# Optimization experiments

Hardware: AMD Instinct MI355X
Metric: run time of the kernel (lower is better)

Reference implementation:

```python
import jax, jax.numpy as jnp
import numpy as np

FEATURE_DIM = 512
Z_DIM = 256
Q_DIM = 128
NUM_Z_CODES = 4096
NUM_Q_CODES = 2048
HIDDEN_DIM = 128 * 4  # 512
BOTTLENECK = 64
BATCH = 32768


def setup_inputs() -> dict:
    key = jax.random.key(0)
    ks = jax.random.split(key, 16)
    d = {}
    d['x'] = jax.random.normal(ks[0], (BATCH, FEATURE_DIM), dtype=jnp.float32)
    # encoder: Linear(feature_dim,64) -> GELU -> Linear(64,hidden) -> GELU
    d['eW1'] = jax.random.normal(ks[1], (BOTTLENECK, FEATURE_DIM), dtype=jnp.float32) * (1.0 / np.sqrt(FEATURE_DIM))
    d['eb1'] = jnp.zeros((BOTTLENECK,), jnp.float32)
    d['eW2'] = jax.random.normal(ks[2], (HIDDEN_DIM, BOTTLENECK), dtype=jnp.float32) * (1.0 / np.sqrt(BOTTLENECK))
    d['eb2'] = jnp.zeros((HIDDEN_DIM,), jnp.float32)
    # to_z_latent LipschitzMLP(hidden, z_dim)
    d['zW'] = jax.random.normal(ks[3], (Z_DIM, HIDDEN_DIM), dtype=jnp.float32) * (1.0 / np.sqrt(HIDDEN_DIM))
    d['zb'] = jnp.zeros((Z_DIM,), jnp.float32)
    d['zci'] = jnp.ones((Z_DIM,), jnp.float32)
    # z codebook
    d['z_codebook'] = jax.random.normal(ks[4], (NUM_Z_CODES, Z_DIM), dtype=jnp.float32)
    # q_encoder LipschitzMLP(z_dim, q_dim)
    d['qW'] = jax.random.normal(ks[5], (Q_DIM, Z_DIM), dtype=jnp.float32) * (1.0 / np.sqrt(Z_DIM))
    d['qb'] = jnp.zeros((Q_DIM,), jnp.float32)
    d['qci'] = jnp.ones((Q_DIM,), jnp.float32)
    # q codebook
    d['q_codebook'] = jax.random.normal(ks[6], (NUM_Q_CODES, Q_DIM), dtype=jnp.float32)
    # decoder: Linear(q_dim,64) -> GELU -> Linear(64,hidden) -> GELU
    d['dW1'] = jax.random.normal(ks[7], (BOTTLENECK, Q_DIM), dtype=jnp.float32) * (1.0 / np.sqrt(Q_DIM))
    d['db1'] = jnp.zeros((BOTTLENECK,), jnp.float32)
    d['dW2'] = jax.random.normal(ks[8], (HIDDEN_DIM, BOTTLENECK), dtype=jnp.float32) * (1.0 / np.sqrt(BOTTLENECK))
    d['db2'] = jnp.zeros((HIDDEN_DIM,), jnp.float32)
    # to_output Linear(hidden, feature_dim)
    d['oW'] = jax.random.normal(ks[9], (FEATURE_DIM, HIDDEN_DIM), dtype=jnp.float32) * (1.0 / np.sqrt(HIDDEN_DIM))
    d['ob'] = jnp.zeros((FEATURE_DIM,), jnp.float32)
    return d


def _gelu(x):
    return jax.nn.gelu(x, approximate=False)  # torch nn.GELU default (erf)


def _lipschitz_mlp(x, W, b, ci):
    # normalization: scale each row of W so its L1 norm <= softplus(ci)
    absrowsum = jnp.sum(jnp.abs(W), axis=1, keepdims=True)          # [out,1]
    scale = jnp.minimum(1.0, jax.nn.softplus(ci)[:, None] / absrowsum)
    W_norm = W * scale
    return jax.nn.sigmoid(x @ W_norm.T + b)


def _quantize(z_e, codebook):
    # ||a-b||^2 = ||a||^2 + ||b||^2 - 2 a.b ; single big GEMM
    z_norm = jnp.sum(z_e * z_e, axis=1, keepdims=True)              # [B,1]
    cb_norm = jnp.sum(codebook * codebook, axis=1)[None, :]         # [1,K]
    dists = z_norm + cb_norm - 2.0 * (z_e @ codebook.T)             # [B,K]
    idx = jnp.argmin(dists, axis=1)
    z_q = codebook[idx]
    return z_q, idx


def _mse(a, b):
    return jnp.mean((a - b) ** 2)


def reference(x, eW1, eb1, eW2, eb2, zW, zb, zci, z_codebook,
              qW, qb, qci, q_codebook, dW1, db1, dW2, db2, oW, ob):
    sg = jax.lax.stop_gradient
    # encoder
    h = _gelu(_gelu(x @ eW1.T + eb1) @ eW2.T + eb2)                 # [B,hidden]
    z_e = _lipschitz_mlp(h, zW, zb, zci)                            # [B,z_dim]
    z_q, z_idx = _quantize(z_e, z_codebook)
    commit_z = _mse(z_e, sg(z_q))
    codebook_z = _mse(z_q, sg(z_e))
    # q level
    q_e = _lipschitz_mlp(sg(z_q), qW, qb, qci)                      # [B,q_dim]
    q_q, q_idx = _quantize(q_e, q_codebook)
    commit_q = _mse(q_e, sg(q_q))
    codebook_q = _mse(q_q, sg(q_e))
    # decoder
    dec_h = _gelu(_gelu(q_q @ dW1.T + db1) @ dW2.T + db2)           # [B,hidden]
    x_recon = dec_h @ oW.T + ob                                     # [B,feature]
    recon_loss = _mse(x_recon, x)
    loss = recon_loss + 0.25 * (commit_z + codebook_z) + 0.25 * (commit_q + codebook_q)
    return (loss, recon_loss, commit_z, codebook_z, commit_q, codebook_q,
            x_recon, z_q, q_q, z_idx, q_idx)
```

## Files before the change

### kernel.cpp

```cpp
#include <hip/hip_runtime.h>

typedef unsigned long long u64;
typedef unsigned short u16;
typedef unsigned int u32;


namespace {

constexpr int kBatch = 32768;

__device__ __forceinline__ float gelu_f(float x) {
  return 0.5f * x * (1.0f + erff(x * 0.70710678118654752440f));
}
__device__ __forceinline__ float sigmoid_f(float x) {
  return 1.0f / (1.0f + expf(-x));
}
__device__ __forceinline__ u64 pack_key(float d, unsigned j) {
  unsigned u = __float_as_uint(d);
  u = (u & 0x80000000u) ? ~u : (u | 0x80000000u);
  return ((u64)u << 32) | j;
}
__device__ __forceinline__ u16 bf16_rne(float x) {
  unsigned u = __float_as_uint(x);
  unsigned r = (u + 0x7FFFu + ((u >> 16) & 1u)) >> 16;
  return (u16)r;
}
__device__ __forceinline__ float bf16_to_f(u16 h) {
  return __uint_as_float((unsigned)h << 16);
}
__device__ __forceinline__ u64 min64(u64 a, u64 b) { return a < b ? a : b; }

__device__ __forceinline__ void load_lds16(const void* g, void* l) {
  __builtin_amdgcn_global_load_lds(
      (const __attribute__((address_space(1))) void*)g,
      (__attribute__((address_space(3))) void*)l, 16, 0, 0);
}

template <int N>
__device__ __forceinline__ void wait_vmcnt() {
  if constexpr (N == 0) {
    asm volatile("s_waitcnt vmcnt(0)" ::: "memory");
  } else if constexpr (N == 1) {
    asm volatile("s_waitcnt vmcnt(1)" ::: "memory");
  } else if constexpr (N == 2) {
    asm volatile("s_waitcnt vmcnt(2)" ::: "memory");
  } else if constexpr (N == 8) {
    asm volatile("s_waitcnt vmcnt(8)" ::: "memory");
  } else if constexpr (N == 16) {
    asm volatile("s_waitcnt vmcnt(16)" ::: "memory");
  }
}

__device__ __forceinline__ void lds_fence_barrier_pre() {
  asm volatile("s_waitcnt lgkmcnt(0)" ::: "memory");
  __builtin_amdgcn_sched_barrier(0);
  __builtin_amdgcn_s_barrier();
  asm volatile("" ::: "memory");
  __builtin_amdgcn_sched_barrier(0);
}

__device__ __forceinline__ void barrier_raw() {
  __builtin_amdgcn_sched_barrier(0);
  __builtin_amdgcn_s_barrier();
  asm volatile("" ::: "memory");
  __builtin_amdgcn_sched_barrier(0);
}

typedef short bf16x8 __attribute__((ext_vector_type(8)));
typedef float f32x4 __attribute__((ext_vector_type(4)));

__global__ void prep_cb_kernel(const float* __restrict__ zcb,
                               u16* __restrict__ zcbh, float* __restrict__ zcbn,
                               const float* __restrict__ qcb,
                               u16* __restrict__ qcbh, float* __restrict__ qcbn) {
  int b = blockIdx.x;
  const float* cb;
  u16* cbh;
  float* cbn;
  int K;
  if (b < 1024) { cb = zcb; cbh = zcbh; cbn = zcbn; K = 256; }
  else { b -= 1024; cb = qcb; cbh = qcbh; cbn = qcbn; K = 128; }
  const int row = b * 4 + (threadIdx.x >> 6);
  const int lane = threadIdx.x & 63;
  double s = 0.0;
  for (int k = lane; k < K; k += 64) {
    const float v = cb[(size_t)row * K + k];
    cbh[(size_t)row * K + k] = bf16_rne(v);
    s += (double)v * (double)v;
  }
#pragma unroll
  for (int o = 32; o > 0; o >>= 1) s += __shfl_down(s, o);
  if (lane == 0) cbn[row] = (float)s;
}

__global__ void prep_w_kernel(
    const float* __restrict__ zW, const float* __restrict__ zci,
    const float* __restrict__ qW, const float* __restrict__ qci,
    const float* __restrict__ eW1, const float* __restrict__ eW2,
    u16* __restrict__ zWns, u16* __restrict__ qWns, u16* __restrict__ eW1s,
    u16* __restrict__ eW2s, const float* __restrict__ dW1,
    const float* __restrict__ dW2, const float* __restrict__ oW,
    u16* __restrict__ dW1b, u16* __restrict__ dW2b, u16* __restrict__ oWb) {
  const int b = blockIdx.x;
  const int tid = threadIdx.x;
  if (b < 384) {
    const float* W;
    const float* ci;
    u16* D;
    int K, row;
    if (b < 256) { W = zW; ci = zci; D = zWns; K = 512; row = b; }
    else { W = qW; ci = qci; D = qWns; K = 256; row = b - 256; }
    float s = 0.f;
    for (int k = tid; k < K; k += 256) s += fabsf(W[(size_t)row * K + k]);
#pragma unroll
    for (int o = 32; o > 0; o >>= 1) s += __shfl_down(s, o);
    __shared__ float p[4];
    if ((tid & 63) == 0) p[tid >> 6] = s;
    __syncthreads();
    const float tot = p[0] + p[1] + p[2] + p[3];
    const float c = ci[row];
    const float sp = (c > 20.f) ? c : log1pf(expf(c));
    const float scale = fminf(1.f, sp / tot);
    for (int k = tid; k < K; k += 256) {
      const float v = W[(size_t)row * K + k] * scale;
      const u16 h = bf16_rne(v);
      const u16 l = bf16_rne(v - bf16_to_f(h));
      D[(size_t)row * 3 * K + k] = h;
      D[(size_t)row * 3 * K + K + k] = h;
      D[(size_t)row * 3 * K + 2 * K + k] = l;
    }
  } else if (b < 512) {
    const int i = (b - 384) * 256 + tid;
    const int r = i >> 9, k = i & 511;
    const float v = eW1[i];
    const u16 h = bf16_rne(v);
    const u16 l = bf16_rne(v - bf16_to_f(h));
    eW1s[(size_t)r * 1536 + k] = h;
    eW1s[(size_t)r * 1536 + 512 + k] = h;
    eW1s[(size_t)r * 1536 + 1024 + k] = l;
  } else if (b < 640) {
    const int i = (b - 512) * 256 + tid;
    const int r = i >> 6, k = i & 63;
    const float v = eW2[i];
    const u16 h = bf16_rne(v);
    const u16 l = bf16_rne(v - bf16_to_f(h));
    eW2s[(size_t)r * 192 + k] = h;
    eW2s[(size_t)r * 192 + 64 + k] = h;
    eW2s[(size_t)r * 192 + 128 + k] = l;
  } else if (b < 672) {
    const int i = (b - 640) * 256 + tid;
    dW1b[i] = bf16_rne(dW1[i]);
  } else if (b < 800) {
    const int i = (b - 672) * 256 + tid;
    dW2b[i] = bf16_rne(dW2[i]);
  } else {
    const int i = (b - 800) * 256 + tid;
    oWb[i] = bf16_rne(oW[i]);
  }
}

__global__ void cast_split_x_kernel(const float* __restrict__ x,
                                    u16* __restrict__ xs) {
  const int i = blockIdx.x * 256 + threadIdx.x;
  const int row = i >> 7, c4 = i & 127;
  const float4 v = *(const float4*)(x + (size_t)row * 512 + c4 * 4);
  const float vv[4] = {v.x, v.y, v.z, v.w};
  u16 hv[4], lv[4];
#pragma unroll
  for (int j = 0; j < 4; ++j) {
    hv[j] = bf16_rne(vv[j]);
    lv[j] = bf16_rne(vv[j] - bf16_to_f(hv[j]));
  }
  *(ushort4*)(xs + (size_t)row * 1024 + c4 * 4) =
      make_ushort4(hv[0], hv[1], hv[2], hv[3]);
  *(ushort4*)(xs + (size_t)row * 1024 + 512 + c4 * 4) =
      make_ushort4(lv[0], lv[1], lv[2], lv[3]);
}

enum { U_GELU_SPLIT = 0, U_SIG_SPLIT = 1, U_GELU_B16 = 2, U_RECON = 3 };

template <int TM, int TN, int NW, int MODE>
__global__ __launch_bounds__(NW * 64) void gemm_uni(
    const u16* __restrict__ A, const u16* __restrict__ B,
    const float* __restrict__ bias, void* __restrict__ Cv,
    const float* __restrict__ X, float* __restrict__ psum, int Ktot,
    int wrapA, int strideA, int N) {
  __shared__ __align__(16) u16 As[TM * 64];
  __shared__ __align__(16) u16 Bs[TN * 64];
  constexpr int NT = NW * 64;
  constexpr int AIT = (TM * 8) / NT;
  constexpr int BIT = (TN * 8) / NT;
  const int tid = threadIdx.x;
  const int lane = tid & 63, w = tid >> 6;
  const int quad = lane >> 4, l15 = lane & 15;
  const int waveM = (TN == 64) ? w * 64 : (w & 1) * 64;
  const int waveN = (TN == 64) ? 0 : (w >> 1) * 64;
  const int rowBase = blockIdx.y * TM;
  const int colBase = blockIdx.x * TN;

  f32x4 acc[4][4] = {};

  for (int k0 = 0; k0 < Ktot; k0 += 64) {
    const int sk0 = (k0 >= wrapA) ? k0 - wrapA : k0;
    __syncthreads();
#pragma unroll
    for (int i = 0; i < AIT; ++i) {
      const int ch = i * NT + tid;
      const int r = ch >> 3, c = ch & 7, g = c ^ (r & 7);
      load_lds16(A + (size_t)(rowBase + r) * strideA + sk0 + g * 8,
                 (char*)As + ch * 16);
    }
#pragma unroll
    for (int i = 0; i < BIT; ++i) {
      const int ch = i * NT + tid;
      const int r = ch >> 3, c = ch & 7, g = c ^ (r & 7);
      load_lds16(B + (size_t)(colBase + r) * Ktot + k0 + g * 8,
                 (char*)Bs + ch * 16);
    }
    __syncthreads();
#pragma unroll
    for (int ks = 0; ks < 2; ++ks) {
      bf16x8 af[4], bf[4];
      const int ch = ks * 4 + quad;
#pragma unroll
      for (int mi = 0; mi < 4; ++mi) {
        const int rl = waveM + mi * 16 + l15;
        af[mi] = *(const bf16x8*)(As + rl * 64 + (ch ^ (rl & 7)) * 8);
      }
#pragma unroll
      for (int ni = 0; ni < 4; ++ni) {
        const int rl = waveN + ni * 16 + l15;
        bf[ni] = *(const bf16x8*)(Bs + rl * 64 + (ch ^ (rl & 7)) * 8);
      }
#pragma unroll
      for (int mi = 0; mi < 4; ++mi)
#pragma unroll
        for (int ni = 0; ni < 4; ++ni)
          acc[mi][ni] = __builtin_amdgcn_mfma_f32_16x16x32_bf16(
              af[mi], bf[ni], acc[mi][ni], 0, 0, 0);
    }
  }

  if constexpr (MODE == U_GELU_SPLIT || MODE == U_SIG_SPLIT) {
    u16* S = (u16*)Cv;
#pragma unroll
    for (int mi = 0; mi < 4; ++mi)
#pragma unroll
      for (int r = 0; r < 4; ++r) {
        const int row = rowBase + waveM + mi * 16 + quad * 4 + r;
#pragma unroll
        for (int ni = 0; ni < 4; ++ni) {
          const int col = colBase + waveN + ni * 16 + l15;
          const float pre = acc[mi][ni][r] + bias[col];
          const float v = (MODE == U_GELU_SPLIT) ? gelu_f(pre) : sigmoid_f(pre);
          const u16 h = bf16_rne(v);
          const u16 l = bf16_rne(v - bf16_to_f(h));
          S[(size_t)row * 2 * N + col] = h;
          S[(size_t)row * 2 * N + N + col] = l;
        }
      }
  } else if constexpr (MODE == U_GELU_B16) {
    u16* C = (u16*)Cv;
#pragma unroll
    for (int mi = 0; mi < 4; ++mi)
#pragma unroll
      for (int r = 0; r < 4; ++r) {
        const int row = rowBase + waveM + mi * 16 + quad * 4 + r;
#pragma unroll
        for (int ni = 0; ni < 4; ++ni) {
          const int col = colBase + waveN + ni * 16 + l15;
          C[(size_t)row * N + col] =
              bf16_rne(gelu_f(acc[mi][ni][r] + bias[col]));
        }
      }
  } else {
    float* C = (float*)Cv;
    float local = 0.f;
#pragma unroll
    for (int mi = 0; mi < 4; ++mi)
#pragma unroll
      for (int r = 0; r < 4; ++r) {
        const int row = rowBase + waveM + mi * 16 + quad * 4 + r;
#pragma unroll
        for (int ni = 0; ni < 4; ++ni) {
          const int col = colBase + waveN + ni * 16 + l15;
          const float val = acc[mi][ni][r] + bias[col];
          const float d = val - X[(size_t)row * N + col];
          local += d * d;
          C[(size_t)row * N + col] = val;
        }
      }
#pragma unroll
    for (int o = 32; o > 0; o >>= 1) local += __shfl_down(local, o);
    __shared__ float psh[NW];
    if (lane == 0) psh[w] = local;
    __syncthreads();
    if (tid == 0) {
      float t = 0.f;
#pragma unroll
      for (int i = 0; i < NW; ++i) t += psh[i];
      psum[blockIdx.y * gridDim.x + blockIdx.x] = t;
    }
  }
}

template <int KT, int CT, int BR, int BTG>
__global__ __launch_bounds__(256) void dist3z_kernel(
    const u16* __restrict__ CB, const u16* __restrict__ ZB,
    const float* __restrict__ cbn, u32* __restrict__ cand, int strideB,
    int ncand) {
  constexpr int CH = KT / 8;
  constexpr int KSTEPS = KT / 32;
  constexpr int CSLOTS = (CT * CH) / 256;
  constexpr int BSLOTS = (BR * CH) / 256;
  __shared__ __align__(16) u16 bufC[CT * KT];
  __shared__ __align__(16) u16 bufB[BR * KT];
  const int tid = threadIdx.x;
  const int lane = tid & 63, w = tid >> 6;
  const int quad = lane >> 4, l15 = lane & 15;
  const int waveN = w * 32;
  const int ct = blockIdx.y;
  const int btg = blockIdx.x;
  const int codeBase = ct * CT;

  float cnf[2][4];
#pragma unroll
  for (int mi = 0; mi < 2; ++mi)
#pragma unroll
    for (int r = 0; r < 4; ++r)
      cnf[mi][r] =
          cbn[codeBase + mi * 16 + quad * 4 + r] * 512.0f + 131072.0f;
  asm volatile("" ::: "memory");

#pragma unroll
  for (int i = 0; i < CSLOTS; ++i) {
    const int ch = i * 256 + tid;
    const int r = ch / CH, c = ch % CH, g = c ^ (r & 7);
    load_lds16(CB + (size_t)(codeBase + r) * KT + g * 8, (char*)bufC + ch * 16);
  }
  {
    const int rowBase0 = btg * BTG * BR;
#pragma unroll
    for (int i = 0; i < BSLOTS; ++i) {
      const int ch = i * 256 + tid;
      const int r = ch / CH, c = ch % CH, g = c ^ (r & 7);
      load_lds16(ZB + (size_t)(rowBase0 + r) * strideB + g * 8,
                 (char*)bufB + ch * 16);
    }
  }
  wait_vmcnt<0>();
  barrier_raw();

  bf16x8 af[KSTEPS][2];
#pragma unroll
  for (int kk = 0; kk < KSTEPS; ++kk)
#pragma unroll
    for (int mi = 0; mi < 2; ++mi) {
      const int rl = mi * 16 + l15;
      const int sw = (kk * 4 + quad) ^ (rl & 7);
      af[kk][mi] = *(const bf16x8*)(bufC + rl * KT + sw * 8);
    }

#pragma unroll 1
  for (int bt = 0; bt < BTG; ++bt) {
    const int rowBase = (btg * BTG + bt) * BR;

    f32x4 acc[2][2] = {};
#pragma unroll
    for (int kk = 0; kk < KSTEPS; ++kk) {
      bf16x8 bf[2];
#pragma unroll
      for (int ni = 0; ni < 2; ++ni) {
        const int rn = waveN + ni * 16 + l15;
        const int sw = (kk * 4 + quad) ^ (rn & 7);
        bf[ni] = *(const bf16x8*)(bufB + rn * KT + sw * 8);
      }
#pragma unroll
      for (int mi = 0; mi < 2; ++mi)
#pragma unroll
        for (int ni = 0; ni < 2; ++ni)
          acc[mi][ni] = __builtin_amdgcn_mfma_f32_16x16x32_bf16(
              af[kk][mi], bf[ni], acc[mi][ni], 0, 0, 0);
    }

    u32 best[2];
#pragma unroll
    for (int ni = 0; ni < 2; ++ni) {
      u32 b0 = ~0u;
#pragma unroll
      for (int mi = 0; mi < 2; ++mi)
#pragma unroll
        for (int r = 0; r < 4; ++r) {
          const float kf = fmaf(acc[mi][ni][r], -1024.0f, cnf[mi][r]);
          u32 iv = (u32)kf;
          iv = iv > 0xFFFFFu ? 0xFFFFFu : iv;
          const u32 key = (iv << 12) | (codeBase + mi * 16 + quad * 4 + r);
          b0 = min(b0, key);
        }
      b0 = min(b0, (u32)__shfl_xor(b0, 16));
      b0 = min(b0, (u32)__shfl_xor(b0, 32));
      best[ni] = b0;
    }
    lds_fence_barrier_pre();

    if (bt + 1 < BTG) {
      const int rowBaseN = rowBase + BR;
#pragma unroll
      for (int i = 0; i < BSLOTS; ++i) {
        const int ch = i * 256 + tid;
        const int r = ch / CH, c = ch % CH, g = c ^ (r & 7);
        load_lds16(ZB + (size_t)(rowBaseN + r) * strideB + g * 8,
                   (char*)bufB + ch * 16);
      }
    }
    if (quad == 0) {
#pragma unroll
      for (int ni = 0; ni < 2; ++ni) {
        const int row = rowBase + waveN + ni * 16 + l15;
        cand[(size_t)row * ncand + ct] = best[ni];
      }
    }
    wait_vmcnt<2>();
    barrier_raw();
  }
}

template <int KT, int CT, int BR, int BTG>
__global__ __launch_bounds__(256) void dist2z_kernel(
    const u16* __restrict__ CB, const u16* __restrict__ ZB,
    const float* __restrict__ cbn, u32* __restrict__ cand, int strideB,
    int ncand) {
  constexpr int CH = KT / 8;
  constexpr int KSTEPS = KT / 32;
  constexpr int CSLOTS = (CT * CH) / 256;
  constexpr int BSLOTS = (BR * CH) / 256;
  __shared__ __align__(16) u16 bufC[CT * KT];
  __shared__ __align__(16) u16 bufB[BR * KT];
  __shared__ u32 wred[BR * 2];
  const int tid = threadIdx.x;
  const int lane = tid & 63, w = tid >> 6;
  const int quad = lane >> 4, l15 = lane & 15;
  const int waveM = (w & 1) * 32;
  const int waveN = (w >> 1) * 32;
  const int ct = blockIdx.y;
  const int btg = blockIdx.x;
  const int codeBase = ct * CT;

  float cnf[2][4];
#pragma unroll
  for (int mi = 0; mi < 2; ++mi)
#pragma unroll
    for (int r = 0; r < 4; ++r)
      cnf[mi][r] =
          cbn[codeBase + waveM + mi * 16 + quad * 4 + r] * 512.0f + 131072.0f;
  asm volatile("" ::: "memory");

#pragma unroll
  for (int i = 0; i < CSLOTS; ++i) {
    const int ch = i * 256 + tid;
    const int r = ch / CH, c = ch % CH, g = c ^ (r & 7);
    load_lds16(CB + (size_t)(codeBase + r) * KT + g * 8, (char*)bufC + ch * 16);
  }
  {
    const int rowBase0 = btg * BTG * BR;
#pragma unroll
    for (int i = 0; i < BSLOTS; ++i) {
      const int ch = i * 256 + tid;
      const int r = ch / CH, c = ch % CH, g = c ^ (r & 7);
      load_lds16(ZB + (size_t)(rowBase0 + r) * strideB + g * 8,
                 (char*)bufB + ch * 16);
    }
  }
  wait_vmcnt<0>();
  barrier_raw();

  bf16x8 af[KSTEPS][2];
#pragma unroll
  for (int kk = 0; kk < KSTEPS; ++kk)
#pragma unroll
    for (int mi = 0; mi < 2; ++mi) {
      const int rl = waveM + mi * 16 + l15;
      const int sw = (kk * 4 + quad) ^ (rl & 7);
      af[kk][mi] = *(const bf16x8*)(bufC + rl * KT + sw * 8);
    }

#pragma unroll 1
  for (int bt = 0; bt < BTG; ++bt) {
    const int rowBase = (btg * BTG + bt) * BR;

    f32x4 acc[2][2] = {};
#pragma unroll
    for (int kk = 0; kk < KSTEPS; ++kk) {
      bf16x8 bf[2];
#pragma unroll
      for (int ni = 0; ni < 2; ++ni) {
        const int rn = waveN + ni * 16 + l15;
        const int sw = (kk * 4 + quad) ^ (rn & 7);
        bf[ni] = *(const bf16x8*)(bufB + rn * KT + sw * 8);
      }
#pragma unroll
      for (int mi = 0; mi < 2; ++mi)
#pragma unroll
        for (int ni = 0; ni < 2; ++ni)
          acc[mi][ni] = __builtin_amdgcn_mfma_f32_16x16x32_bf16(
              af[kk][mi], bf[ni], acc[mi][ni], 0, 0, 0);
    }

#pragma unroll
    for (int ni = 0; ni < 2; ++ni) {
      u32 b0 = ~0u;
#pragma unroll
      for (int mi = 0; mi < 2; ++mi)
#pragma unroll
        for (int r = 0; r < 4; ++r) {
          const float kf = fmaf(acc[mi][ni][r], -1024.0f, cnf[mi][r]);
          u32 iv = (u32)kf;
          iv = iv > 0xFFFFFu ? 0xFFFFFu : iv;
          const u32 key =
              (iv << 12) | (codeBase + waveM + mi * 16 + quad * 4 + r);
          b0 = min(b0, key);
        }
      b0 = min(b0, (u32)__shfl_xor(b0, 16));
      b0 = min(b0, (u32)__shfl_xor(b0, 32));
      if (quad == 0) {
        const int rloc = waveN + ni * 16 + l15;
        wred[rloc * 2 + (w & 1)] = b0;
      }
    }
    lds_fence_barrier_pre();

    if (bt + 1 < BTG) {
      const int rowBaseN = rowBase + BR;
#pragma unroll
      for (int i = 0; i < BSLOTS; ++i) {
        const int ch = i * 256 + tid;
        const int r = ch / CH, c = ch % CH, g = c ^ (r & 7);
        load_lds16(ZB + (size_t)(rowBaseN + r) * strideB + g * 8,
                   (char*)bufB + ch * 16);
      }
    }
    if (tid < BR) {
      const u32 m0 = min(wred[tid * 2 + 0], wred[tid * 2 + 1]);
      cand[(size_t)(rowBase + tid) * ncand + ct] = m0;
    }
    wait_vmcnt<1>();
    lds_fence_barrier_pre();
  }
}

template <int K, int NC, int LEVEL>
__global__ __launch_bounds__(256, 4) void rerank_kernel(
    const u32* __restrict__ cand, const u16* __restrict__ zes,
    const float* __restrict__ cb, const float* __restrict__ cbn,
    float* __restrict__ outq, u16* __restrict__ wsq,
    float* __restrict__ out_idx, float* __restrict__ psum) {
  constexpr int DV = K / 32;
  constexpr int MV = K / 64;
  constexpr int NK = (NC + 63) / 64;
  const int w = threadIdx.x >> 6, lane = threadIdx.x & 63;
  const int row = blockIdx.x * 4 + w;
  const int g = lane >> 3, sub = lane & 7;

  const u16* zr = zes + (size_t)row * 2 * K;

  ushort4 zh[DV], zl[DV];
#pragma unroll
  for (int i = 0; i < DV; ++i) {
    zh[i] = *(const ushort4*)(zr + sub * (K / 8) + 4 * i);
    zl[i] = *(const ushort4*)(zr + K + sub * (K / 8) + 4 * i);
  }
  float zmse[MV];
#pragma unroll
  for (int i = 0; i < MV; ++i) {
    const int c = lane + 64 * i;
    zmse[i] = bf16_to_f(zr[c]) + bf16_to_f(zr[K + c]);
  }
  u32 mk0 = (lane < NC) ? cand[(size_t)row * NC + lane] : ~0u;
  u32 mk1 = (NK == 2) ? cand[(size_t)row * NC + 64 + lane] : ~0u;

  unsigned topcode[8];
#pragma unroll
  for (int t = 0; t < 8; ++t) {
    u32 m = min(mk0, mk1);
#pragma unroll
    for (int off = 1; off < 64; off <<= 1) m = min(m, (u32)__shfl_xor(m, off));
    topcode[t] = m & 0xFFFu;
    if (mk0 == m) mk0 = ~0u;
    else if (mk1 == m) mk1 = ~0u;
  }
  unsigned ci = topcode[0];
#pragma unroll
  for (int t = 1; t < 8; ++t) ci = (g == t) ? topcode[t] : ci;

  const float* cr = cb + (size_t)ci * K;
  float dot = 0.f;
#pragma unroll
  for (int i = 0; i < DV; ++i) {
    const float4 cv = *(const float4*)(cr + sub * (K / 8) + 4 * i);
    dot = fmaf(bf16_to_f(zh[i].x) + bf16_to_f(zl[i].x), cv.x, dot);
    dot = fmaf(bf16_to_f(zh[i].y) + bf16_to_f(zl[i].y), cv.y, dot);
    dot = fmaf(bf16_to_f(zh[i].z) + bf16_to_f(zl[i].z), cv.z, dot);
    dot = fmaf(bf16_to_f(zh[i].w) + bf16_to_f(zl[i].w), cv.w, dot);
  }
#pragma unroll
  for (int off = 1; off < 8; off <<= 1) dot += __shfl_xor(dot, off);
  u64 k2 = pack_key(cbn[ci] - 2.0f * dot, ci);
#pragma unroll
  for (int off = 8; off < 64; off <<= 1) k2 = min64(k2, __shfl_xor(k2, off));
  const unsigned best = (unsigned)k2;
  if (lane == 0) out_idx[row] = (float)best;

  const float* br = cb + (size_t)best * K;
  float local = 0.f;
#pragma unroll
  for (int i = 0; i < MV; ++i) {
    const int c = lane + 64 * i;
    const float v = br[c];
    const float d = zmse[i] - v;
    local += d * d;
    outq[(size_t)row * K + c] = v;
    if (LEVEL == 0) {
      const u16 h = bf16_rne(v);
      wsq[(size_t)row * 2 * K + c] = h;
      wsq[(size_t)row * 2 * K + K + c] = bf16_rne(v - bf16_to_f(h));
    } else {
      wsq[(size_t)row * K + c] = bf16_rne(v);
    }
  }
#pragma unroll
  for (int o = 32; o > 0; o >>= 1) local += __shfl_down(local, o);
  __shared__ float p[4];
  if (lane == 0) p[w] = local;
  __syncthreads();
  if (threadIdx.x == 0) psum[blockIdx.x] = p[0] + p[1] + p[2] + p[3];
}

__global__ void finalize_kernel(const float* __restrict__ psumZ,
                                const float* __restrict__ psumQ,
                                const float* __restrict__ psumR,
                                float* __restrict__ out) {
  const int tid = threadIdx.x;
  float sz = 0.f, sq = 0.f, sr = 0.f;
  for (int i = tid; i < 8192; i += 256) {
    sz += psumZ[i];
    sq += psumQ[i];
  }
  for (int i = tid; i < 1024; i += 256) sr += psumR[i];
#pragma unroll
  for (int o = 32; o > 0; o >>= 1) {
    sz += __shfl_down(sz, o);
    sq += __shfl_down(sq, o);
    sr += __shfl_down(sr, o);
  }
  __shared__ float pz[4], pq[4], pr[4];
  if ((tid & 63) == 0) {
    pz[tid >> 6] = sz;
    pq[tid >> 6] = sq;
    pr[tid >> 6] = sr;
  }
  __syncthreads();
  if (tid == 0) {
    const float cz = (pz[0] + pz[1] + pz[2] + pz[3]) / ((float)kBatch * 256.f);
    const float cq = (pq[0] + pq[1] + pq[2] + pq[3]) / ((float)kBatch * 128.f);
    const float rec = (pr[0] + pr[1] + pr[2] + pr[3]) / ((float)kBatch * 512.f);
    out[0] = rec + 0.5f * cz + 0.5f * cq;
    out[1] = rec;
    out[2] = cz;
    out[3] = cz;
    out[4] = cq;
    out[5] = cq;
  }
}

}

extern "C" void kernel_launch(void* const* d_in, const int* in_sizes, int n_in,
                              void* d_out, int out_size, void* d_ws,
                              size_t ws_size, hipStream_t stream) {
  const float* x   = (const float*)d_in[0];
  const float* eW1 = (const float*)d_in[1];
  const float* eb1 = (const float*)d_in[2];
  const float* eW2 = (const float*)d_in[3];
  const float* eb2 = (const float*)d_in[4];
  const float* zW  = (const float*)d_in[5];
  const float* zb  = (const float*)d_in[6];
  const float* zci = (const float*)d_in[7];
  const float* zcb = (const float*)d_in[8];
  const float* qW  = (const float*)d_in[9];
  const float* qb  = (const float*)d_in[10];
  const float* qci = (const float*)d_in[11];
  const float* qcb = (const float*)d_in[12];
  const float* dW1 = (const float*)d_in[13];
  const float* db1 = (const float*)d_in[14];
  const float* dW2 = (const float*)d_in[15];
  const float* db2 = (const float*)d_in[16];
  const float* oW  = (const float*)d_in[17];
  const float* ob  = (const float*)d_in[18];

  float* out = (float*)d_out;
  float* out_xr = out + 6;
  float* out_zq = out_xr + (size_t)32768 * 512;
  float* out_qq = out_zq + (size_t)32768 * 256;
  float* out_zi = out_qq + (size_t)32768 * 128;
  float* out_qi = out_zi + 32768;

  char* wsb = (char*)d_ws;
  u16*  zWns = (u16*) (wsb + 0x0000000);
  u16*  qWns = (u16*) (wsb + 0x00C0000);
  u16*  eW1s = (u16*) (wsb + 0x00F0000);
  u16*  eW2s = (u16*) (wsb + 0x0120000);
  u16*  dW1b = (u16*) (wsb + 0x0150000);
  u16*  dW2b = (u16*) (wsb + 0x0154000);
  u16*  oWb  = (u16*) (wsb + 0x0164000);
  u16*  zcbh = (u16*) (wsb + 0x01E4000);
  u16*  qcbh = (u16*) (wsb + 0x03E4000);
  float* zcbn = (float*)(wsb + 0x0464000);
  float* qcbn = (float*)(wsb + 0x0468000);
  float* psumR = (float*)(wsb + 0x046B000);
  float* psumZ = (float*)(wsb + 0x0470000);
  float* psumQ = (float*)(wsb + 0x0478000);
  u16*  h1s  = (u16*) (wsb + 0x0480000);
  u16*  h1b  = (u16*) (wsb + 0x0480000);
  u16*  zes  = (u16*) (wsb + 0x0C80000);
  u16*  qes  = (u16*) (wsb + 0x0C80000);
  u16*  hb   = (u16*) (wsb + 0x0C80000);
  u16*  xs   = (u16*) (wsb + 0x2C80000);
  u16*  hs   = (u16*) (wsb + 0x2C80000);
  u32*  candq = (u32*)(wsb + 0x2C80000);
  u16*  zqs  = (u16*) (wsb + 0x3480000);
  u16*  qqb  = (u16*) (wsb + 0x5480000);
  u32*  candz = (u32*)(wsb + 0x5C80000);

  prep_cb_kernel<<<1536, 256, 0, stream>>>(zcb, zcbh, zcbn, qcb, qcbh, qcbn);
  prep_w_kernel<<<1824, 256, 0, stream>>>(zW, zci, qW, qci, eW1, eW2, zWns,
                                          qWns, eW1s, eW2s, dW1, dW2, oW,
                                          dW1b, dW2b, oWb);
  cast_split_x_kernel<<<16384, 256, 0, stream>>>(x, xs);

  gemm_uni<128, 64, 2, U_GELU_SPLIT><<<dim3(1, 256), 128, 0, stream>>>(
      xs, eW1s, eb1, h1s, nullptr, nullptr, 1536, 1024, 1024, 64);
  gemm_uni<128, 128, 4, U_GELU_SPLIT><<<dim3(4, 256), 256, 0, stream>>>(
      h1s, eW2s, eb2, hs, nullptr, nullptr, 192, 128, 128, 512);
  gemm_uni<128, 128, 4, U_SIG_SPLIT><<<dim3(2, 256), 256, 0, stream>>>(
      hs, zWns, zb, zes, nullptr, nullptr, 1536, 1024, 1024, 256);

  dist3z_kernel<256, 32, 128, 32><<<dim3(8, 128), 256, 0, stream>>>(
      zcbh, zes, zcbn, candz, 512, 128);
  rerank_kernel<256, 128, 0><<<8192, 256, 0, stream>>>(
      candz, zes, zcb, zcbn, out_zq, zqs, out_zi, psumZ);

  gemm_uni<128, 128, 4, U_SIG_SPLIT><<<dim3(1, 256), 256, 0, stream>>>(
      zqs, qWns, qb, qes, nullptr, nullptr, 768, 512, 512, 128);
  dist2z_kernel<128, 64, 64, 16><<<dim3(32, 32), 256, 0, stream>>>(
      qcbh, qes, qcbn, candq, 256, 32);
  rerank_kernel<128, 32, 1><<<8192, 256, 0, stream>>>(
      candq, qes, qcb, qcbn, out_qq, qqb, out_qi, psumQ);

  gemm_uni<128, 64, 2, U_GELU_B16><<<dim3(1, 256), 128, 0, stream>>>(
      qqb, dW1b, db1, h1b, nullptr, nullptr, 128, 1 << 30, 128, 64);
  gemm_uni<128, 128, 4, U_GELU_B16><<<dim3(4, 256), 256, 0, stream>>>(
      h1b, dW2b, db2, hb, nullptr, nullptr, 64, 1 << 30, 64, 512);
  gemm_uni<128, 128, 4, U_RECON><<<dim3(4, 256), 256, 0, stream>>>(
      hb, oWb, ob, out_xr, x, psumR, 512, 1 << 30, 512, 512);

  finalize_kernel<<<1, 256, 0, stream>>>(psumZ, psumQ, psumR, out);

  (void)in_sizes; (void)n_in; (void)out_size; (void)ws_size;
}
```

Baseline: 703.4 us.

## Retile z distance kernel to 64-code tiles and rank-sort top-8 candidates

The z-level distance kernel now uses 64-code tiles split across wave pairs and 32-row batch tiles, with a shared-memory min-reduction. This halves the per-row candidate count from 128 to 64. The rerank kernel replaces eight iterative wave-wide min-reductions with a single LDS-based rank computation to pick the top 8 candidates. The candidate buffer is moved to reuse an earlier workspace region. Fewer candidates changes how well the coarse bf16 shortlist covers the true nearest code, and the rerank top-8 now relies on LDS traffic and block syncs.

```diff
diff --git a/kernel.cpp b/kernel.cpp
--- a/kernel.cpp
+++ b/kernel.cpp
@@ -42,8 +42,6 @@
     asm volatile("s_waitcnt vmcnt(0)" ::: "memory");
   } else if constexpr (N == 1) {
     asm volatile("s_waitcnt vmcnt(1)" ::: "memory");
-  } else if constexpr (N == 2) {
-    asm volatile("s_waitcnt vmcnt(2)" ::: "memory");
   } else if constexpr (N == 8) {
     asm volatile("s_waitcnt vmcnt(8)" ::: "memory");
   } else if constexpr (N == 16) {
@@ -305,7 +303,7 @@
 }
 
 template <int KT, int CT, int BR, int BTG>
-__global__ __launch_bounds__(256) void dist3z_kernel(
+__global__ __launch_bounds__(256) void dist4z_kernel(
     const u16* __restrict__ CB, const u16* __restrict__ ZB,
     const float* __restrict__ cbn, u32* __restrict__ cand, int strideB,
     int ncand) {
@@ -315,10 +313,12 @@
   constexpr int BSLOTS = (BR * CH) / 256;
   __shared__ __align__(16) u16 bufC[CT * KT];
   __shared__ __align__(16) u16 bufB[BR * KT];
+  __shared__ u32 wred[BR * 2];
   const int tid = threadIdx.x;
   const int lane = tid & 63, w = tid >> 6;
   const int quad = lane >> 4, l15 = lane & 15;
-  const int waveN = w * 32;
+  const int waveM = (w & 1) * 32;
+  const int waveN = (w >> 1) * 16;
   const int ct = blockIdx.y;
   const int btg = blockIdx.x;
   const int codeBase = ct * CT;
@@ -329,7 +329,7 @@
 #pragma unroll
     for (int r = 0; r < 4; ++r)
       cnf[mi][r] =
-          cbn[codeBase + mi * 16 + quad * 4 + r] * 512.0f + 131072.0f;
+          cbn[codeBase + waveM + mi * 16 + quad * 4 + r] * 512.0f + 131072.0f;
   asm volatile("" ::: "memory");
 
 #pragma unroll
@@ -356,7 +356,7 @@
   for (int kk = 0; kk < KSTEPS; ++kk)
 #pragma unroll
     for (int mi = 0; mi < 2; ++mi) {
-      const int rl = mi * 16 + l15;
+      const int rl = waveM + mi * 16 + l15;
       const int sw = (kk * 4 + quad) ^ (rl & 7);
       af[kk][mi] = *(const bf16x8*)(bufC + rl * KT + sw * 8);
     }
@@ -365,41 +365,40 @@
   for (int bt = 0; bt < BTG; ++bt) {
     const int rowBase = (btg * BTG + bt) * BR;
 
-    f32x4 acc[2][2] = {};
+    f32x4 acc[2] = {};
 #pragma unroll
     for (int kk = 0; kk < KSTEPS; ++kk) {
-      bf16x8 bf[2];
-#pragma unroll
-      for (int ni = 0; ni < 2; ++ni) {
-        const int rn = waveN + ni * 16 + l15;
+      bf16x8 bf;
+      {
+        const int rn = waveN + l15;
         const int sw = (kk * 4 + quad) ^ (rn & 7);
-        bf[ni] = *(const bf16x8*)(bufB + rn * KT + sw * 8);
+        bf = *(const bf16x8*)(bufB + rn * KT + sw * 8);
       }
 #pragma unroll
       for (int mi = 0; mi < 2; ++mi)
-#pragma unroll
-        for (int ni = 0; ni < 2; ++ni)
-          acc[mi][ni] = __builtin_amdgcn_mfma_f32_16x16x32_bf16(
-              af[kk][mi], bf[ni], acc[mi][ni], 0, 0, 0);
-    }
-
-    u32 best[2];
-#pragma unroll
-    for (int ni = 0; ni < 2; ++ni) {
+        acc[mi] = __builtin_amdgcn_mfma_f32_16x16x32_bf16(
+            af[kk][mi], bf, acc[mi], 0, 0, 0);
+    }
+
+    {
       u32 b0 = ~0u;
 #pragma unroll
       for (int mi = 0; mi < 2; ++mi)
 #pragma unroll
         for (int r = 0; r < 4; ++r) {
-          const float kf = fmaf(acc[mi][ni][r], -1024.0f, cnf[mi][r]);
+          const float kf = fmaf(acc[mi][r], -1024.0f, cnf[mi][r]);
           u32 iv = (u32)kf;
           iv = iv > 0xFFFFFu ? 0xFFFFFu : iv;
-          const u32 key = (iv << 12) | (codeBase + mi * 16 + quad * 4 + r);
+          const u32 key =
+              (iv << 12) | (codeBase + waveM + mi * 16 + quad * 4 + r);
           b0 = min(b0, key);
         }
       b0 = min(b0, (u32)__shfl_xor(b0, 16));
       b0 = min(b0, (u32)__shfl_xor(b0, 32));
-      best[ni] = b0;
+      if (quad == 0) {
+        const int rloc = waveN + l15;
+        wred[rloc * 2 + (w & 1)] = b0;
+      }
     }
     lds_fence_barrier_pre();
 
@@ -413,15 +412,12 @@
                    (char*)bufB + ch * 16);
       }
     }
-    if (quad == 0) {
-#pragma unroll
-      for (int ni = 0; ni < 2; ++ni) {
-        const int row = rowBase + waveN + ni * 16 + l15;
-        cand[(size_t)row * ncand + ct] = best[ni];
-      }
-    }
-    wait_vmcnt<2>();
-    barrier_raw();
+    if (tid < BR) {
+      const u32 m0 = min(wred[tid * 2 + 0], wred[tid * 2 + 1]);
+      cand[(size_t)(rowBase + tid) * ncand + ct] = m0;
+    }
+    wait_vmcnt<1>();
+    lds_fence_barrier_pre();
   }
 }
 
@@ -556,7 +552,6 @@
     float* __restrict__ out_idx, float* __restrict__ psum) {
   constexpr int DV = K / 32;
   constexpr int MV = K / 64;
-  constexpr int NK = (NC + 63) / 64;
   const int w = threadIdx.x >> 6, lane = threadIdx.x & 63;
   const int row = blockIdx.x * 4 + w;
   const int g = lane >> 3, sub = lane & 7;
@@ -575,22 +570,20 @@
     const int c = lane + 64 * i;
     zmse[i] = bf16_to_f(zr[c]) + bf16_to_f(zr[K + c]);
   }
-  u32 mk0 = (lane < NC) ? cand[(size_t)row * NC + lane] : ~0u;
-  u32 mk1 = (NK == 2) ? cand[(size_t)row * NC + 64 + lane] : ~0u;
-
-  unsigned topcode[8];
-#pragma unroll
-  for (int t = 0; t < 8; ++t) {
-    u32 m = min(mk0, mk1);
-#pragma unroll
-    for (int off = 1; off < 64; off <<= 1) m = min(m, (u32)__shfl_xor(m, off));
-    topcode[t] = m & 0xFFFu;
-    if (mk0 == m) mk0 = ~0u;
-    else if (mk1 == m) mk1 = ~0u;
-  }
-  unsigned ci = topcode[0];
-#pragma unroll
-  for (int t = 1; t < 8; ++t) ci = (g == t) ? topcode[t] : ci;
+  const u32 mykey = (lane < NC) ? cand[(size_t)row * NC + lane] : ~0u;
+
+  __shared__ u32 kb[4][72];
+  kb[w][lane] = mykey;
+  __syncthreads();
+  int rank = 0;
+#pragma unroll
+  for (int j = 0; j < 64; ++j) {
+    const u32 kj = kb[w][j];
+    rank += (kj < mykey || (kj == mykey && j < lane)) ? 1 : 0;
+  }
+  if (rank < 8) kb[w][64 + rank] = mykey;
+  __syncthreads();
+  const unsigned ci = kb[w][64 + g] & 0xFFFu;
 
   const float* cr = cb + (size_t)ci * K;
   float dot = 0.f;
@@ -726,10 +719,10 @@
   u16*  hb   = (u16*) (wsb + 0x0C80000);
   u16*  xs   = (u16*) (wsb + 0x2C80000);
   u16*  hs   = (u16*) (wsb + 0x2C80000);
+  u32*  candz = (u32*)(wsb + 0x2C80000);
+  u16*  zqs  = (u16*) (wsb + 0x3480000);
   u32*  candq = (u32*)(wsb + 0x2C80000);
-  u16*  zqs  = (u16*) (wsb + 0x3480000);
   u16*  qqb  = (u16*) (wsb + 0x5480000);
-  u32*  candz = (u32*)(wsb + 0x5C80000);
 
   prep_cb_kernel<<<1536, 256, 0, stream>>>(zcb, zcbh, zcbn, qcb, qcbh, qcbn);
   prep_w_kernel<<<1824, 256, 0, stream>>>(zW, zci, qW, qci, eW1, eW2, zWns,
@@ -744,9 +737,9 @@
   gemm_uni<128, 128, 4, U_SIG_SPLIT><<<dim3(2, 256), 256, 0, stream>>>(
       hs, zWns, zb, zes, nullptr, nullptr, 1536, 1024, 1024, 256);
 
-  dist3z_kernel<256, 32, 128, 32><<<dim3(8, 128), 256, 0, stream>>>(
-      zcbh, zes, zcbn, candz, 512, 128);
-  rerank_kernel<256, 128, 0><<<8192, 256, 0, stream>>>(
+  dist4z_kernel<256, 64, 32, 64><<<dim3(16, 64), 256, 0, stream>>>(
+      zcbh, zes, zcbn, candz, 512, 64);
+  rerank_kernel<256, 64, 0><<<8192, 256, 0, stream>>>(
       candz, zes, zcb, zcbn, out_zq, zqs, out_zi, psumZ);
 
   gemm_uni<128, 128, 4, U_SIG_SPLIT><<<dim3(1, 256), 256, 0, stream>>>(
```

Result: faster. 675.8 us (-3.9%).
